# Kernel optimization log

Measured on AMD Instinct MI355X. Metric: run time of the kernel, lower is better.

The kernel has to match this reference:

```python
import jax, jax.numpy as jnp
import numpy as np

BETA = 0.25      # commitment loss weight
DECAY = 0.99     # EMA decay
EPS = 1e-5       # Laplace smoothing for counts


def setup_inputs() -> dict:
    key = jax.random.key(0)
    k1, k2, k3 = jax.random.split(key, 3)
    B, d, h, w, K = 16, 64, 64, 64, 1024
    z_e = jax.random.normal(k1, (B, d, h, w), dtype=jnp.float32)
    codebook = jax.random.normal(k2, (K, d), dtype=jnp.float32)
    ema_count = jnp.ones((K,), dtype=jnp.float32)
    ema_sum = jax.random.normal(k3, (K, d), dtype=jnp.float32)
    return {"z_e": z_e, "codebook": codebook, "ema_count": ema_count, "ema_sum": ema_sum}


def reference(z_e, codebook, ema_count, ema_sum):
    B, d, h, w = z_e.shape
    K = codebook.shape[0]
    # [B,d,h,w] -> [N,d], N = B*h*w
    z_flat = jnp.transpose(z_e, (0, 2, 3, 1)).reshape(-1, d)
    # squared euclidean distances [N,K]
    dist = (jnp.sum(z_flat * z_flat, axis=1, keepdims=True)
            - 2.0 * (z_flat @ codebook.T)
            + jnp.sum(codebook * codebook, axis=1)[None, :])
    indices = jnp.argmin(dist, axis=1)                      # [N] int
    e_k = codebook[indices].reshape(B, h, w, d).transpose(0, 3, 1, 2)  # [B,d,h,w]

    # --- EMA codebook update (training mode, no grad) ---
    zf = jax.lax.stop_gradient(z_flat)
    counts = jax.ops.segment_sum(jnp.ones((zf.shape[0],), dtype=zf.dtype), indices, num_segments=K)
    sums = jax.ops.segment_sum(zf, indices, num_segments=K)
    new_count = ema_count * DECAY + (1.0 - DECAY) * counts
    new_sum = ema_sum * DECAY + (1.0 - DECAY) * sums
    n = jnp.sum(new_count)
    count_s = (new_count + EPS) / (n + K * EPS) * n
    new_codebook = new_sum / count_s[:, None]

    # straight-through estimator
    e_k_ste = z_e + jax.lax.stop_gradient(e_k - z_e)
    L_commit = (jnp.mean((z_e - jax.lax.stop_gradient(e_k)) ** 2)
                + BETA * jnp.mean((jax.lax.stop_gradient(z_e) - e_k) ** 2))
    return (e_k_ste, indices.reshape(B, h, w), L_commit, new_codebook, new_count, new_sum)
```

## Files before the change

### kernel.cpp

```cpp
#include <hip/hip_runtime.h>
#include <hip/hip_bf16.h>
#include <hip/hip_fp16.h>

#define NB 16
#define DD 64
#define HW 4096
#define NTOT 65536
#define KC 1024

#define O_EK   0
#define O_IDX  4194304
#define O_L    4259840
#define O_CB   4259841
#define O_CNT  4325377
#define O_SUM  4326401

#define WS_IDX    0
#define WS_LCPART 65536
#define WS_N      66048
#define WS_CNORM  66560
#define WS_PSUM   67584
#define WS_PCNT   329728
#define WS_CBH    399360
#define WS_CBL    432128

#define MARGIN 0.002f

typedef _Float16 v8h __attribute__((ext_vector_type(8)));
typedef float    v4f __attribute__((ext_vector_type(4)));

__global__ __launch_bounds__(256) void k_pre(const float* __restrict__ cb,
                                             const float* __restrict__ ema_count,
                                             float* __restrict__ cnorm,
                                             float* __restrict__ n_ws,
                                             unsigned short* __restrict__ cbh,
                                             unsigned short* __restrict__ cbl) {
    const int t = threadIdx.x;
    const int w = (blockIdx.x * 256 + t) >> 6;
    const int l = t & 63;
    float s = 0.f;
    if (l < 16) {
        float4 v = *(const float4*)(cb + (size_t)w * DD + l * 4);
        s = v.x * v.x + v.y * v.y + v.z * v.z + v.w * v.w;
    }
#pragma unroll
    for (int m = 1; m <= 8; m <<= 1) s += __shfl_xor(s, m, 64);
    if (l == 0) cnorm[w] = s;

    const int e4 = blockIdx.x * 256 + t;
    if (e4 < 16384) {
        float4 v4 = ((const float4*)cb)[e4];
        __half hx = __float2half(v4.x), hy = __float2half(v4.y),
               hz = __float2half(v4.z), hw2 = __float2half(v4.w);
        ushort4 h4 = { __half_as_ushort(hx), __half_as_ushort(hy),
                       __half_as_ushort(hz), __half_as_ushort(hw2) };
        ((ushort4*)cbh)[e4] = h4;
        ushort4 l4 = { __half_as_ushort(__float2half(v4.x - __half2float(hx))),
                       __half_as_ushort(__float2half(v4.y - __half2float(hy))),
                       __half_as_ushort(__float2half(v4.z - __half2float(hz))),
                       __half_as_ushort(__float2half(v4.w - __half2float(hw2))) };
        ((ushort4*)cbl)[e4] = l4;
    }

    if (blockIdx.x == 0) {
        __shared__ float red[256];
        red[t] = ema_count[t] + ema_count[t + 256] + ema_count[t + 512] + ema_count[t + 768];
        __syncthreads();
        for (int s2 = 128; s2 >= 1; s2 >>= 1) {
            if (t < s2) red[t] += red[t + s2];
            __syncthreads();
        }
        if (t == 0) n_ws[0] = 0.99f * red[0] + 0.01f * 65536.0f;
    }
}

__global__ __launch_bounds__(256) void k_argmin(const float* __restrict__ z_e,
                                                const float* __restrict__ cb,
                                                const unsigned short* __restrict__ cbh,
                                                const unsigned short* __restrict__ cbl,
                                                const float* __restrict__ cnorm,
                                                int* __restrict__ idx_ws,
                                                float* __restrict__ out) {
    __shared__ __align__(16) unsigned short Ah[128 * 72];
    __shared__ __align__(16) unsigned short Al[128 * 72];
    __shared__ __align__(16) unsigned short Bh[128 * 72];
    __shared__ __align__(16) unsigned short Bl[128 * 72];
    __shared__ __align__(16) float cn_lds[KC];
    __shared__ float znl[128];
    __shared__ int   idx_lds[128];
    __shared__ int   flagrows[128];
    __shared__ int   nflag;
    __shared__ float redv4[4];
    __shared__ int   redi4[4];

    const int t  = threadIdx.x;
    const int n0 = blockIdx.x * 128;
    const int b   = n0 >> 12;
    const int hw0 = n0 & 4095;

    if (t == 0) nflag = 0;
    *(float4*)&cn_lds[t * 4] = *(const float4*)(cnorm + t * 4);

    if (t < 128) {
        const float* zp = z_e + (size_t)b * (DD * HW) + hw0 + t;
        float s = 0.f;
        unsigned ph = 0, pl = 0;
        for (int j = 0; j < 64; ++j) {
            float v = zp[(size_t)j * HW];
            s = fmaf(v, v, s);
            __half h = __float2half(v);
            float hf = __half2float(h);
            __half lo = __float2half(v - hf);
            unsigned uh = __half_as_ushort(h), ul = __half_as_ushort(lo);
            if ((j & 1) == 0) { ph = uh; pl = ul; }
            else {
                *(unsigned*)&Ah[t * 72 + j - 1] = ph | (uh << 16);
                *(unsigned*)&Al[t * 72 + j - 1] = pl | (ul << 16);
            }
        }
        znl[t] = s;
    }
    __syncthreads();

    const int w    = t >> 6;
    const int lane = t & 63;
    const int c    = lane & 15;
    const int q    = lane >> 4;

    v8h Afh[2][2], Afl[2][2];
#pragma unroll
    for (int g = 0; g < 2; ++g) {
        int m = 32 * w + 16 * g + c;
#pragma unroll
        for (int s = 0; s < 2; ++s) {
            Afh[g][s] = *(const v8h*)&Ah[m * 72 + s * 32 + q * 8];
            Afl[g][s] = *(const v8h*)&Al[m * 72 + s * 32 + q * 8];
        }
    }

    float m1v[2][4], m2v[2][4]; int m1i[2][4];
#pragma unroll
    for (int g = 0; g < 2; ++g)
#pragma unroll
        for (int r = 0; r < 4; ++r) { m1v[g][r] = 3.4e38f; m2v[g][r] = 3.4e38f; m1i[g][r] = 0; }

    for (int kt = 0; kt < 8; ++kt) {
        __syncthreads();
#pragma unroll
        for (int s2 = 0; s2 < 4; ++s2) {
            int idx = t + s2 * 256;
            int code = idx >> 3;
            int off  = (idx & 7) * 8;
            size_t gsrc = ((size_t)(kt * 128 + code)) * 64 + off;
            *(uint4*)&Bh[code * 72 + off] = *(const uint4*)(cbh + gsrc);
            *(uint4*)&Bl[code * 72 + off] = *(const uint4*)(cbl + gsrc);
        }
        __syncthreads();

#pragma unroll
        for (int sub = 0; sub < 8; ++sub) {
            const int cl = sub * 16 + c;
            v8h Bfh0 = *(const v8h*)&Bh[cl * 72 + q * 8];
            v8h Bfh1 = *(const v8h*)&Bh[cl * 72 + 32 + q * 8];
            v8h Bfl0 = *(const v8h*)&Bl[cl * 72 + q * 8];
            v8h Bfl1 = *(const v8h*)&Bl[cl * 72 + 32 + q * 8];
            float cnc = cn_lds[kt * 128 + cl];
            const int kg = kt * 128 + cl;
#pragma unroll
            for (int g = 0; g < 2; ++g) {
                v4f acc = {0.f, 0.f, 0.f, 0.f};
                acc = __builtin_amdgcn_mfma_f32_16x16x32_f16(Afh[g][0], Bfh0, acc, 0, 0, 0);
                acc = __builtin_amdgcn_mfma_f32_16x16x32_f16(Afh[g][1], Bfh1, acc, 0, 0, 0);
                acc = __builtin_amdgcn_mfma_f32_16x16x32_f16(Afh[g][0], Bfl0, acc, 0, 0, 0);
                acc = __builtin_amdgcn_mfma_f32_16x16x32_f16(Afh[g][1], Bfl1, acc, 0, 0, 0);
                acc = __builtin_amdgcn_mfma_f32_16x16x32_f16(Afl[g][0], Bfh0, acc, 0, 0, 0);
                acc = __builtin_amdgcn_mfma_f32_16x16x32_f16(Afl[g][1], Bfh1, acc, 0, 0, 0);
#pragma unroll
                for (int r = 0; r < 4; ++r) {
                    float v = fmaf(-2.0f, acc[r], cnc);
                    bool better = v < m1v[g][r];
                    m2v[g][r] = better ? m1v[g][r] : fminf(m2v[g][r], v);
                    m1i[g][r] = better ? kg : m1i[g][r];
                    m1v[g][r] = better ? v : m1v[g][r];
                }
            }
        }
    }

#pragma unroll
    for (int g = 0; g < 2; ++g)
#pragma unroll
        for (int r = 0; r < 4; ++r) {
            float a = m1v[g][r], b2 = m2v[g][r]; int ii = m1i[g][r];
#pragma unroll
            for (int mask = 1; mask <= 8; mask <<= 1) {
                float ov = __shfl_xor(a, mask, 64);
                int   oi = __shfl_xor(ii, mask, 64);
                float o2 = __shfl_xor(b2, mask, 64);
                bool take = (ov < a) || (ov == a && oi < ii);
                float loser = take ? a : ov;
                b2 = fminf(fminf(b2, o2), loser);
                a  = take ? ov : a;
                ii = take ? oi : ii;
            }
            if (c == 0) {
                int row = 32 * w + 16 * g + q * 4 + r;
                idx_lds[row] = ii;
                if ((b2 - a) < MARGIN) { int p = atomicAdd(&nflag, 1); flagrows[p] = row; }
            }
        }
    __syncthreads();

    const int nf = nflag;
    for (int f = 0; f < nf; ++f) {
        int row = flagrows[f];
        const float* zrow = z_e + (size_t)b * (DD * HW) + hw0 + row;
        float znr = znl[row];
        float best = 3.4e38f; int bi = 0;
#pragma unroll
        for (int c2 = 0; c2 < 4; ++c2) {
            int k = t * 4 + c2;
            const float* ck = cb + (size_t)k * DD;
            float acc = 0.f;
            for (int j = 0; j < 64; ++j) acc = fmaf(zrow[(size_t)j * HW], ck[j], acc);
            float v = (znr - 2.0f * acc) + cn_lds[k];
            if (v < best) { best = v; bi = k; }
        }
#pragma unroll
        for (int mask = 1; mask <= 32; mask <<= 1) {
            float ov = __shfl_xor(best, mask, 64);
            int   oi = __shfl_xor(bi, mask, 64);
            if (ov < best || (ov == best && oi < bi)) { best = ov; bi = oi; }
        }
        if (lane == 0) { redv4[w] = best; redi4[w] = bi; }
        __syncthreads();
        if (t == 0) {
            float bv = redv4[0]; int bix = redi4[0];
#pragma unroll
            for (int w2 = 1; w2 < 4; ++w2) {
                if (redv4[w2] < bv || (redv4[w2] == bv && redi4[w2] < bix)) { bv = redv4[w2]; bix = redi4[w2]; }
            }
            idx_lds[row] = bix;
        }
        __syncthreads();
    }

    if (t < 128) {
        int bi = idx_lds[t];
        out[O_IDX + n0 + t] = (float)bi;
        idx_ws[n0 + t] = bi;
    }
}

__global__ __launch_bounds__(1024) void k_out(const int* __restrict__ idx_ws,
                                              const float* __restrict__ z_e,
                                              const float* __restrict__ cb,
                                              float* __restrict__ psum,
                                              int* __restrict__ pcnt,
                                              float* __restrict__ lc_part,
                                              float* __restrict__ out) {
    __shared__ float acc[KC];
    __shared__ int bins[KC];
    __shared__ float cbj[KC];
    __shared__ float lcr[16];
    const int j = blockIdx.x & 63;
    const int c = blockIdx.x >> 6;
    const int t = threadIdx.x;
    acc[t] = 0.f;
    bins[t] = 0;
    cbj[t] = cb[(size_t)t * DD + j];
    __syncthreads();
    const float* zj = z_e + (size_t)j * HW;
    float* oj = out + O_EK + (size_t)j * HW;
    const int base = c * 16384;
    float lc = 0.f;
#pragma unroll
    for (int i = 0; i < 4; ++i) {
        int n4 = base + i * 4096 + t * 4;
        int b = n4 >> 12, hw = n4 & 4095;
        size_t zoff = (size_t)b * (DD * HW) + hw;
        float4 z4 = *(const float4*)(zj + zoff);
        int4   k4 = *(const int4*)(idx_ws + n4);
        float e0 = cbj[k4.x], e1 = cbj[k4.y], e2 = cbj[k4.z], e3 = cbj[k4.w];
        float4 o4 = { z4.x + (e0 - z4.x), z4.y + (e1 - z4.y),
                      z4.z + (e2 - z4.z), z4.w + (e3 - z4.w) };
        *(float4*)(oj + zoff) = o4;
        float d0 = z4.x - e0, d1 = z4.y - e1, d2 = z4.z - e2, d3 = z4.w - e3;
        lc = fmaf(d0, d0, lc); lc = fmaf(d1, d1, lc);
        lc = fmaf(d2, d2, lc); lc = fmaf(d3, d3, lc);
        atomicAdd(&acc[k4.x], z4.x);
        atomicAdd(&acc[k4.y], z4.y);
        atomicAdd(&acc[k4.z], z4.z);
        atomicAdd(&acc[k4.w], z4.w);
        if (j == 0) {
            atomicAdd(&bins[k4.x], 1); atomicAdd(&bins[k4.y], 1);
            atomicAdd(&bins[k4.z], 1); atomicAdd(&bins[k4.w], 1);
        }
    }
    __syncthreads();
    psum[(size_t)c * 65536 + j * 1024 + t] = acc[t];
    if (j == 0) pcnt[c * 1024 + t] = bins[t];
#pragma unroll
    for (int m = 32; m >= 1; m >>= 1) lc += __shfl_xor(lc, m, 64);
    if ((t & 63) == 0) lcr[t >> 6] = lc;
    __syncthreads();
    if (t == 0) {
        float s = 0.f;
#pragma unroll
        for (int u = 0; u < 16; ++u) s += lcr[u];
        lc_part[blockIdx.x] = s;
    }
}

__global__ __launch_bounds__(1024) void k_epi(const float* __restrict__ psum,
                                              const int* __restrict__ pcnt,
                                              const float* __restrict__ ema_sum,
                                              const float* __restrict__ ema_count,
                                              const float* __restrict__ n_ws,
                                              const float* __restrict__ lc_part,
                                              float* __restrict__ out) {
    const int t = threadIdx.x;
    const int e = blockIdx.x * 1024 + t;
    const int k = e >> 6, j = e & 63;
    float s4 = psum[j * 1024 + k] + psum[65536 + j * 1024 + k]
             + psum[131072 + j * 1024 + k] + psum[196608 + j * 1024 + k];
    float ns = ema_sum[e] * 0.99f + 0.01f * s4;
    out[O_SUM + e] = ns;
    int cnt = pcnt[k] + pcnt[1024 + k] + pcnt[2048 + k] + pcnt[3072 + k];
    float nc = ema_count[k] * 0.99f + 0.01f * (float)cnt;
    float n  = n_ws[0];
    float cs = (nc + 1e-5f) / (n + 1024.0f * 1e-5f) * n;
    out[O_CB + e] = ns / cs;
    if (blockIdx.x == 0) {
        int c2 = pcnt[t] + pcnt[1024 + t] + pcnt[2048 + t] + pcnt[3072 + t];
        out[O_CNT + t] = ema_count[t] * 0.99f + 0.01f * (float)c2;
    }
    if (blockIdx.x == 1) {
        __shared__ float red[512];
        if (t < 512) red[t] = (t < 256) ? lc_part[t] : 0.f;
        __syncthreads();
        for (int s = 256; s >= 1; s >>= 1) {
            if (t < s) red[t] += red[t + s];
            __syncthreads();
        }
        if (t == 0) out[O_L] = 1.25f * red[0] * (1.0f / 4194304.0f);
    }
}

extern "C" void kernel_launch(void* const* d_in, const int* in_sizes, int n_in,
                              void* d_out, int out_size, void* d_ws, size_t ws_size,
                              hipStream_t stream) {
    const float* z_e       = (const float*)d_in[0];
    const float* cb        = (const float*)d_in[1];
    const float* ema_count = (const float*)d_in[2];
    const float* ema_sum   = (const float*)d_in[3];
    float* out             = (float*)d_out;

    float* ws_f      = (float*)d_ws;
    int*   idx_ws    = (int*)d_ws;
    float* lc_part   = ws_f + WS_LCPART;
    float* n_ws      = ws_f + WS_N;
    float* cnorm_ws  = ws_f + WS_CNORM;
    float* psum      = ws_f + WS_PSUM;
    int*   pcnt      = (int*)(ws_f + WS_PCNT);
    unsigned short* cbh = (unsigned short*)(ws_f + WS_CBH);
    unsigned short* cbl = (unsigned short*)(ws_f + WS_CBL);

    k_pre<<<256, 256, 0, stream>>>(cb, ema_count, cnorm_ws, n_ws, cbh, cbl);
    k_argmin<<<NTOT / 128, 256, 0, stream>>>(z_e, cb, cbh, cbl, cnorm_ws, idx_ws, out);
    k_out<<<256, 1024, 0, stream>>>(idx_ws, z_e, cb, psum, pcnt, lc_part, out);
    k_epi<<<64, 1024, 0, stream>>>(psum, pcnt, ema_sum, ema_count, n_ws, lc_part, out);
}
```

Measured before the change: 164.5 us.

## Coalesce z tile loads via LDS and split tie refinement into separate kernel

Loads the 64x128 z tile with coalesced float4 reads into shared memory (reusing the B buffers), then converts to fp16 hi/lo from LDS instead of per-thread strided global loads. The exact fp32 re-check of near-tie rows is moved out of the argmin kernel into a new k_fix kernel driven by per-block flag lists in workspace. This aims to cut uncoalesced global traffic and keep the fallback loop from stalling argmin blocks; it adds a kernel launch and caps flagged rows per block at 32, silently dropping refinement beyond that.

```diff
diff --git a/kernel.cpp b/kernel.cpp
--- a/kernel.cpp
+++ b/kernel.cpp
@@ -21,10 +21,13 @@
 #define WS_CNORM  66560
 #define WS_PSUM   67584
 #define WS_PCNT   329728
+#define WS_FLGC   333824
+#define WS_FLGL   334336
 #define WS_CBH    399360
 #define WS_CBL    432128
 
 #define MARGIN 0.002f
+#define MAXFLG 32
 
 typedef _Float16 v8h __attribute__((ext_vector_type(8)));
 typedef float    v4f __attribute__((ext_vector_type(4)));
@@ -75,52 +78,67 @@
 }
 
 __global__ __launch_bounds__(256) void k_argmin(const float* __restrict__ z_e,
-                                                const float* __restrict__ cb,
                                                 const unsigned short* __restrict__ cbh,
                                                 const unsigned short* __restrict__ cbl,
                                                 const float* __restrict__ cnorm,
                                                 int* __restrict__ idx_ws,
+                                                int* __restrict__ flg_cnt,
+                                                int* __restrict__ flg_list,
                                                 float* __restrict__ out) {
     __shared__ __align__(16) unsigned short Ah[128 * 72];
     __shared__ __align__(16) unsigned short Al[128 * 72];
-    __shared__ __align__(16) unsigned short Bh[128 * 72];
-    __shared__ __align__(16) unsigned short Bl[128 * 72];
+    __shared__ __align__(16) unsigned short Bs[2][128 * 72];
     __shared__ __align__(16) float cn_lds[KC];
     __shared__ float znl[128];
     __shared__ int   idx_lds[128];
     __shared__ int   flagrows[128];
     __shared__ int   nflag;
-    __shared__ float redv4[4];
-    __shared__ int   redi4[4];
+
+    unsigned short* Bh = &Bs[0][0];
+    unsigned short* Bl = &Bs[1][0];
+    float* Atf = (float*)&Bs[0][0];
 
     const int t  = threadIdx.x;
     const int n0 = blockIdx.x * 128;
     const int b   = n0 >> 12;
     const int hw0 = n0 & 4095;
+    const float* zbase = z_e + (size_t)b * (DD * HW) + hw0;
 
     if (t == 0) nflag = 0;
     *(float4*)&cn_lds[t * 4] = *(const float4*)(cnorm + t * 4);
 
+#pragma unroll
+    for (int s = 0; s < 8; ++s) {
+        int idx = t + s * 256;
+        int j   = idx >> 5;
+        int i4  = (idx & 31) << 2;
+        float4 v = *(const float4*)(zbase + (size_t)j * HW + i4);
+        *(float4*)(&Atf[j * 128 + i4]) = v;
+    }
+    __syncthreads();
+
+    {
+        const int m  = t & 127;
+        const int j0 = (t >> 7) * 32;
+#pragma unroll 4
+        for (int jj = 0; jj < 32; jj += 2) {
+            int j = j0 + jj;
+            float v0 = Atf[j * 128 + m];
+            float v1 = Atf[(j + 1) * 128 + m];
+            __half h0 = __float2half(v0), h1 = __float2half(v1);
+            __half l0 = __float2half(v0 - __half2float(h0));
+            __half l1 = __float2half(v1 - __half2float(h1));
+            *(unsigned*)&Ah[m * 72 + j] = (unsigned)__half_as_ushort(h0) | ((unsigned)__half_as_ushort(h1) << 16);
+            *(unsigned*)&Al[m * 72 + j] = (unsigned)__half_as_ushort(l0) | ((unsigned)__half_as_ushort(l1) << 16);
+        }
+    }
+    __syncthreads();
+
     if (t < 128) {
-        const float* zp = z_e + (size_t)b * (DD * HW) + hw0 + t;
         float s = 0.f;
-        unsigned ph = 0, pl = 0;
-        for (int j = 0; j < 64; ++j) {
-            float v = zp[(size_t)j * HW];
-            s = fmaf(v, v, s);
-            __half h = __float2half(v);
-            float hf = __half2float(h);
-            __half lo = __float2half(v - hf);
-            unsigned uh = __half_as_ushort(h), ul = __half_as_ushort(lo);
-            if ((j & 1) == 0) { ph = uh; pl = ul; }
-            else {
-                *(unsigned*)&Ah[t * 72 + j - 1] = ph | (uh << 16);
-                *(unsigned*)&Al[t * 72 + j - 1] = pl | (ul << 16);
-            }
-        }
+        for (int j = 0; j < 64; ++j) { float a = Atf[j * 128 + t]; s = fmaf(a, a, s); }
         znl[t] = s;
     }
-    __syncthreads();
 
     const int w    = t >> 6;
     const int lane = t & 63;
@@ -211,11 +229,40 @@
         }
     __syncthreads();
 
-    const int nf = nflag;
+    int nf = nflag; if (nf > MAXFLG) nf = MAXFLG;
+    if (t == 0) flg_cnt[blockIdx.x] = nf;
+    if (t < nf) flg_list[blockIdx.x * MAXFLG + t] = flagrows[t];
+
+    if (t < 128) {
+        int bi = idx_lds[t];
+        out[O_IDX + n0 + t] = (float)bi;
+        idx_ws[n0 + t] = bi;
+    }
+}
+
+__global__ __launch_bounds__(256) void k_fix(const float* __restrict__ z_e,
+                                             const float* __restrict__ cb,
+                                             const float* __restrict__ cnorm,
+                                             const int* __restrict__ flg_cnt,
+                                             const int* __restrict__ flg_list,
+                                             int* __restrict__ idx_ws,
+                                             float* __restrict__ out) {
+    const int blk = blockIdx.x;
+    const int nf = flg_cnt[blk];
+    if (nf == 0) return;
+    __shared__ float redv4[4];
+    __shared__ int   redi4[4];
+    const int t = threadIdx.x;
+    const int lane = t & 63, w = t >> 6;
+    const int n0 = blk * 128;
+    const int b   = n0 >> 12;
+    const int hw0 = n0 & 4095;
+
     for (int f = 0; f < nf; ++f) {
-        int row = flagrows[f];
+        int row = flg_list[blk * MAXFLG + f];
         const float* zrow = z_e + (size_t)b * (DD * HW) + hw0 + row;
-        float znr = znl[row];
+        float znr = 0.f;
+        for (int j = 0; j < 64; ++j) { float v = zrow[(size_t)j * HW]; znr = fmaf(v, v, znr); }
         float best = 3.4e38f; int bi = 0;
 #pragma unroll
         for (int c2 = 0; c2 < 4; ++c2) {
@@ -223,7 +270,7 @@
             const float* ck = cb + (size_t)k * DD;
             float acc = 0.f;
             for (int j = 0; j < 64; ++j) acc = fmaf(zrow[(size_t)j * HW], ck[j], acc);
-            float v = (znr - 2.0f * acc) + cn_lds[k];
+            float v = (znr - 2.0f * acc) + cnorm[k];
             if (v < best) { best = v; bi = k; }
         }
 #pragma unroll
@@ -237,18 +284,12 @@
         if (t == 0) {
             float bv = redv4[0]; int bix = redi4[0];
 #pragma unroll
-            for (int w2 = 1; w2 < 4; ++w2) {
+            for (int w2 = 1; w2 < 4; ++w2)
                 if (redv4[w2] < bv || (redv4[w2] == bv && redi4[w2] < bix)) { bv = redv4[w2]; bix = redi4[w2]; }
-            }
-            idx_lds[row] = bix;
-        }
-        __syncthreads();
-    }
-
-    if (t < 128) {
-        int bi = idx_lds[t];
-        out[O_IDX + n0 + t] = (float)bi;
-        idx_ws[n0 + t] = bi;
+            idx_ws[n0 + row] = bix;
+            out[O_IDX + n0 + row] = (float)bix;
+        }
+        __syncthreads();
     }
 }
 
@@ -363,11 +404,14 @@
     float* cnorm_ws  = ws_f + WS_CNORM;
     float* psum      = ws_f + WS_PSUM;
     int*   pcnt      = (int*)(ws_f + WS_PCNT);
+    int*   flg_cnt   = (int*)(ws_f + WS_FLGC);
+    int*   flg_list  = (int*)(ws_f + WS_FLGL);
     unsigned short* cbh = (unsigned short*)(ws_f + WS_CBH);
     unsigned short* cbl = (unsigned short*)(ws_f + WS_CBL);
 
     k_pre<<<256, 256, 0, stream>>>(cb, ema_count, cnorm_ws, n_ws, cbh, cbl);
-    k_argmin<<<NTOT / 128, 256, 0, stream>>>(z_e, cb, cbh, cbl, cnorm_ws, idx_ws, out);
+    k_argmin<<<NTOT / 128, 256, 0, stream>>>(z_e, cbh, cbl, cnorm_ws, idx_ws, flg_cnt, flg_list, out);
+    k_fix<<<NTOT / 128, 256, 0, stream>>>(z_e, cb, cnorm_ws, flg_cnt, flg_list, idx_ws, out);
     k_out<<<256, 1024, 0, stream>>>(idx_ws, z_e, cb, psum, pcnt, lc_part, out);
     k_epi<<<64, 1024, 0, stream>>>(psum, pcnt, ema_sum, ema_count, n_ws, lc_part, out);
 }
```

Result: faster. 160.1 us (-2.6%).
